# Performance work log

Measured on AMD Instinct MI355X. Metric: run time of the kernel, lower is better.

Reference implementation:

```python
import jax, jax.numpy as jnp
import numpy as np

B, S, D = 4, 2048, 1024
H = 16
HD = D // H  # 64


def setup_inputs() -> dict:
    key = jax.random.key(0)
    ks = jax.random.split(key, 8)
    scale = 1.0 / np.sqrt(D)
    return {
        "hidden_states": jax.random.normal(ks[0], (B, S, D), dtype=jnp.float32),
        "attention_mask": jnp.ones((B, 1, 1, S), dtype=jnp.int32),
        "Wq": jax.random.normal(ks[1], (D, D), dtype=jnp.float32) * scale,
        "bq": jax.random.normal(ks[2], (D,), dtype=jnp.float32) * 0.02,
        "Wk": jax.random.normal(ks[3], (D, D), dtype=jnp.float32) * scale,
        "bk": jax.random.normal(ks[4], (D,), dtype=jnp.float32) * 0.02,
        "Wv": jax.random.normal(ks[5], (D, D), dtype=jnp.float32) * scale,
        "bv": jax.random.normal(ks[6], (D,), dtype=jnp.float32) * 0.02,
    }


def _split_heads(x):
    # [b, t, (h d)] -> [b, h, t, d]
    b, t, _ = x.shape
    return x.reshape(b, t, H, HD).transpose(0, 2, 1, 3)


def reference(hidden_states, attention_mask, Wq, bq, Wk, bk, Wv, bv):
    # Linear projections (torch Linear: x @ W.T + b)
    q = _split_heads(hidden_states @ Wq.T + bq)
    k = _split_heads(hidden_states @ Wk.T + bk)
    v = _split_heads(hidden_states @ Wv.T + bv)

    # scaled dot-product scores: [b, h, s, s]
    scores = jnp.einsum("bhqd,bhkd->bhqk", q, k) / np.sqrt(HD)

    s = scores.shape[-1]
    causal = jnp.tril(jnp.ones((s, s), dtype=bool))[None, None]
    neg_inf = jnp.float32(-jnp.inf)
    scores = jnp.where(causal, scores, neg_inf)
    # attention_mask is 0/1 keep mask: [b, 1, 1, s]
    scores = jnp.where(attention_mask == 0, neg_inf, scores)

    probs = jax.nn.softmax(scores, axis=-1)  # dropout p=0 (eval)
    ctx = jnp.einsum("bhqk,bhkd->bhqd", probs, v)
    # [b, h, t, d] -> [b, t, h*d]
    return ctx.transpose(0, 2, 1, 3).reshape(hidden_states.shape[0], s, D)
```

## Files before the change

kernel.cpp:

```cpp
#include <hip/hip_runtime.h>
#include <hip/hip_bf16.h>
#include <math.h>


#define B_ 4
#define S_ 2048
#define D_ 1024
#define H_ 16
#define HD_ 64
#define M_ (B_ * S_)

typedef unsigned short u16;
typedef unsigned int u32;
typedef __attribute__((ext_vector_type(4))) float f32x4;
typedef __attribute__((ext_vector_type(8))) short bf16x8;

__device__ __forceinline__ u16 f2bfu_rn(float x) {
    u32 u = __builtin_bit_cast(u32, x);
    return (u16)((u + 0x8000u) >> 16);
}

__device__ __forceinline__ void gl2lds16(const void* g, void* l) {
    __builtin_amdgcn_global_load_lds(
        (const __attribute__((address_space(1))) u32*)g,
        (__attribute__((address_space(3))) u32*)l, 16, 0, 0);
}

#define XN  8388608u
#define WN  1048576u
__global__ __launch_bounds__(256) void convert_bf16(
    const float* __restrict__ X,  const float* __restrict__ Wq,
    const float* __restrict__ Wk, const float* __restrict__ Wv,
    u16* __restrict__ Xb, u16* __restrict__ Wqb,
    u16* __restrict__ Wkb, u16* __restrict__ Wvb)
{
    size_t idx = ((size_t)blockIdx.x * 256 + threadIdx.x) * 8;
    const float* src; u16* dst; size_t off;
    if (idx < XN)                { src = X;  dst = Xb;  off = idx; }
    else if (idx < XN + WN)      { src = Wq; dst = Wqb; off = idx - XN; }
    else if (idx < XN + 2 * WN)  { src = Wk; dst = Wkb; off = idx - XN - WN; }
    else                         { src = Wv; dst = Wvb; off = idx - XN - 2 * WN; }
    float4 a = *(const float4*)(src + off);
    float4 b = *(const float4*)(src + off + 4);
    uint4 o;
    o.x = (u32)f2bfu_rn(a.x) | ((u32)f2bfu_rn(a.y) << 16);
    o.y = (u32)f2bfu_rn(a.z) | ((u32)f2bfu_rn(a.w) << 16);
    o.z = (u32)f2bfu_rn(b.x) | ((u32)f2bfu_rn(b.y) << 16);
    o.w = (u32)f2bfu_rn(b.z) | ((u32)f2bfu_rn(b.w) << 16);
    *(uint4*)(dst + off) = o;
}

#define QSCALE 0.18033688011112042f

__global__ __launch_bounds__(256) void qkv_mfma(
    const u16* __restrict__ Xb,
    const u16* __restrict__ Wqb, const u16* __restrict__ Wkb,
    const u16* __restrict__ Wvb,
    const float* __restrict__ bq, const float* __restrict__ bk,
    const float* __restrict__ bv,
    u16* __restrict__ Qb, u16* __restrict__ Kb, u16* __restrict__ Vtb)
{
    const int which = blockIdx.z;
    const u16* Asrc; const u16* Bsrc; const float* bias; u16* Out;
    int m0, n0;
    if (which == 0)      { Asrc = Xb;  Bsrc = Wqb; bias = bq; Out = Qb;
                           m0 = blockIdx.y * 128; n0 = blockIdx.x * 128; }
    else if (which == 1) { Asrc = Xb;  Bsrc = Wkb; bias = bk; Out = Kb;
                           m0 = blockIdx.y * 128; n0 = blockIdx.x * 128; }
    else                 { Asrc = Wvb; Bsrc = Xb;  bias = bv; Out = Vtb;
                           m0 = blockIdx.x * 128; n0 = blockIdx.y * 128; }

    __shared__ u16 As[128][64];
    __shared__ u16 Bs[128][64];

    const int t = threadIdx.x;
    const int wave = t >> 6, lane = t & 63;
    const int qd = lane >> 4, l15 = lane & 15;
    const int wm = wave >> 1, wn = wave & 1;

    const f32x4 zero = {0.f, 0.f, 0.f, 0.f};
    f32x4 acc[4][4];
#pragma unroll
    for (int i = 0; i < 4; ++i)
#pragma unroll
        for (int j = 0; j < 4; ++j) acc[i][j] = zero;

    for (int k0 = 0; k0 < D_; k0 += 64) {
        __syncthreads();
#pragma unroll
        for (int i = 0; i < 4; ++i) {
            int r0  = (wave * 4 + i) * 8;
            int row = r0 + (lane >> 3);
            int g   = (lane & 7) ^ (row & 7);
            gl2lds16(Asrc + (size_t)(m0 + row) * D_ + k0 + g * 8, &As[r0][0]);
            gl2lds16(Bsrc + (size_t)(n0 + row) * D_ + k0 + g * 8, &Bs[r0][0]);
        }
        __syncthreads();
#pragma unroll
        for (int ks = 0; ks < 2; ++ks) {
            bf16x8 af[4], bf[4];
#pragma unroll
            for (int mt = 0; mt < 4; ++mt) {
                int row = wm * 64 + mt * 16 + l15;
                int p = (ks * 4 + qd) ^ (row & 7);
                af[mt] = *(const bf16x8*)&As[row][p * 8];
            }
#pragma unroll
            for (int nt = 0; nt < 4; ++nt) {
                int row = wn * 64 + nt * 16 + l15;
                int p = (ks * 4 + qd) ^ (row & 7);
                bf[nt] = *(const bf16x8*)&Bs[row][p * 8];
            }
#pragma unroll
            for (int mt = 0; mt < 4; ++mt)
#pragma unroll
                for (int nt = 0; nt < 4; ++nt)
                    acc[mt][nt] = __builtin_amdgcn_mfma_f32_16x16x32_bf16(
                        af[mt], bf[nt], acc[mt][nt], 0, 0, 0);
        }
    }

    if (which < 2) {
#pragma unroll
        for (int nt = 0; nt < 4; ++nt) {
            int n = n0 + wn * 64 + nt * 16 + l15;
            float bv_ = bias[n];
            int h = n >> 6, hd = n & 63;
#pragma unroll
            for (int mt = 0; mt < 4; ++mt)
#pragma unroll
                for (int r = 0; r < 4; ++r) {
                    int m = m0 + wm * 64 + mt * 16 + qd * 4 + r;
                    int bb = m >> 11, s = m & 2047;
                    float v = acc[mt][nt][r] + bv_;
                    if (which == 0) v *= QSCALE;
                    Out[(((size_t)(bb * H_ + h)) * S_ + s) * HD_ + hd] = f2bfu_rn(v);
                }
        }
    } else {
#pragma unroll
        for (int mt = 0; mt < 4; ++mt)
#pragma unroll
            for (int r = 0; r < 4; ++r) {
                int f = m0 + wm * 64 + mt * 16 + qd * 4 + r;
                float bv_ = bias[f];
                int h = f >> 6, hd = f & 63;
#pragma unroll
                for (int nt = 0; nt < 4; ++nt) {
                    int tok = n0 + wn * 64 + nt * 16 + l15;
                    int bb = tok >> 11, s = tok & 2047;
                    float v = acc[mt][nt][r] + bv_;
                    Out[(((size_t)(bb * H_ + h)) * HD_ + hd) * S_ + s] = f2bfu_rn(v);
                }
            }
    }
}

__global__ __launch_bounds__(256) void attn_mfma(
    const u16* __restrict__ Qb, const u16* __restrict__ Kb,
    const u16* __restrict__ Vtb, const int* __restrict__ amask,
    float* __restrict__ Out)
{
    const int bh = blockIdx.y;
    const int b = bh >> 4, h = bh & 15;
    const int qt = (int)(gridDim.x - 1) - (int)blockIdx.x;
    const int q0 = qt * 64;
    const int t = threadIdx.x;
    const int wave = t >> 6, lane = t & 63;
    const int qd = lane >> 4, l15 = lane & 15;

    __shared__ u16 Ks[64][64];
    __shared__ u16 Vts[64][64];
    __shared__ u16 Ps[64][72];
    __shared__ float mb[64];

    const size_t base = (size_t)bh * S_ * HD_;
    const u16* Qg = Qb + base;
    const u16* Kg = Kb + base;
    const u16* Vg = Vtb + base;

    bf16x8 qf[2];
    {
        const u16* qrow = Qg + (size_t)(q0 + wave * 16 + l15) * HD_;
        qf[0] = *(const bf16x8*)(qrow + qd * 8);
        qf[1] = *(const bf16x8*)(qrow + 32 + qd * 8);
    }
    bf16x8 onesf;
    {
        short v = (l15 == 0) ? (short)0x3F80 : (short)0;
        onesf = (bf16x8){v, v, v, v, v, v, v, v};
    }

    const f32x4 zero = {0.f, 0.f, 0.f, 0.f};
    f32x4 o[5];
#pragma unroll
    for (int i = 0; i < 5; ++i) o[i] = zero;

    for (int jt = 0; jt <= qt; ++jt) {
        const int j0 = jt * 64;
        __syncthreads();
#pragma unroll
        for (int i = 0; i < 2; ++i) {
            int r0  = (wave * 2 + i) * 8;
            int row = r0 + (lane >> 3);
            int g   = (lane & 7) ^ (row & 7);
            gl2lds16(Kg + (size_t)(j0 + row) * HD_ + g * 8, &Ks[r0][0]);
            gl2lds16(Vg + (size_t)row * S_ + j0 + g * 8, &Vts[r0][0]);
        }
        if (t < 64) mb[t] = (amask[b * S_ + j0 + t] == 0) ? -1e30f : 0.0f;
        __syncthreads();

        f32x4 sacc[4];
#pragma unroll
        for (int nt = 0; nt < 4; ++nt) sacc[nt] = zero;
#pragma unroll
        for (int ks = 0; ks < 2; ++ks) {
#pragma unroll
            for (int nt = 0; nt < 4; ++nt) {
                int brow = nt * 16 + l15;
                int bp = (ks * 4 + qd) ^ (brow & 7);
                bf16x8 bf = *(const bf16x8*)&Ks[brow][bp * 8];
                sacc[nt] = __builtin_amdgcn_mfma_f32_16x16x32_bf16(
                    qf[ks], bf, sacc[nt], 0, 0, 0);
            }
        }

        float bias[4];
#pragma unroll
        for (int nt = 0; nt < 4; ++nt) bias[nt] = mb[nt * 16 + l15];
        const bool diag = (jt == qt);
#pragma unroll
        for (int r = 0; r < 4; ++r) {
            int prow = wave * 16 + qd * 4 + r;
#pragma unroll
            for (int nt = 0; nt < 4; ++nt) {
                int col = nt * 16 + l15;
                float s = sacc[nt][r] + bias[nt];
                if (diag && col > (prow)) s = -1e30f;
                float p = __builtin_amdgcn_exp2f(s);
                Ps[prow][col] = f2bfu_rn(p);
            }
        }

#pragma unroll
        for (int ks = 0; ks < 2; ++ks) {
            int arow = wave * 16 + l15;
            bf16x8 pf = *(const bf16x8*)&Ps[arow][ks * 32 + qd * 8];
#pragma unroll
            for (int nt = 0; nt < 4; ++nt) {
                int brow = nt * 16 + l15;
                int bp = (ks * 4 + qd) ^ (brow & 7);
                bf16x8 vf = *(const bf16x8*)&Vts[brow][bp * 8];
                o[nt] = __builtin_amdgcn_mfma_f32_16x16x32_bf16(
                    pf, vf, o[nt], 0, 0, 0);
            }
            o[4] = __builtin_amdgcn_mfma_f32_16x16x32_bf16(
                pf, onesf, o[4], 0, 0, 0);
        }
    }

#pragma unroll
    for (int r = 0; r < 4; ++r) {
        float l = __shfl(o[4][r], lane & 48);
        float inv = 1.0f / l;
        int q = q0 + wave * 16 + qd * 4 + r;
#pragma unroll
        for (int nt = 0; nt < 4; ++nt) {
            int hd = nt * 16 + l15;
            Out[((size_t)(b * S_ + q)) * D_ + h * HD_ + hd] = o[nt][r] * inv;
        }
    }
}

extern "C" void kernel_launch(void* const* d_in, const int* in_sizes, int n_in,
                              void* d_out, int out_size, void* d_ws, size_t ws_size,
                              hipStream_t stream) {
    (void)in_sizes; (void)n_in; (void)out_size; (void)ws_size;
    const float* X    = (const float*)d_in[0];
    const int*   mask = (const int*)d_in[1];
    const float* Wq   = (const float*)d_in[2];
    const float* bq   = (const float*)d_in[3];
    const float* Wk   = (const float*)d_in[4];
    const float* bk   = (const float*)d_in[5];
    const float* Wv   = (const float*)d_in[6];
    const float* bv   = (const float*)d_in[7];
    float* out = (float*)d_out;

    u16* Xb  = (u16*)d_ws;
    u16* Wqb = Xb  + XN;
    u16* Wkb = Wqb + WN;
    u16* Wvb = Wkb + WN;
    u16* Qb  = Wvb + WN;
    u16* Kb  = Qb  + XN;
    u16* Vtb = Kb  + XN;

    convert_bf16<<<(XN + 3 * WN) / (256 * 8), 256, 0, stream>>>(
        X, Wq, Wk, Wv, Xb, Wqb, Wkb, Wvb);
    qkv_mfma<<<dim3(D_ / 128, M_ / 128, 3), 256, 0, stream>>>(
        Xb, Wqb, Wkb, Wvb, bq, bk, bv, Qb, Kb, Vtb);
    attn_mfma<<<dim3(S_ / 64, B_ * H_), 256, 0, stream>>>(
        Qb, Kb, Vtb, mask, out);
}
```

Before: 281.8 us.

## Load weights directly into registers in QKV GEMM; use 32x32 MFMA 128-row attention tiles

The QKV projection kernel no longer stages the weight tile in shared memory. Each wave loads its weight fragments straight from global memory into registers, and only the token tile goes through LDS; the V path swaps the MFMA operand order to keep its transposed output. The attention kernel now processes 128 query rows per block using 32x32x16 MFMA instructions, so each K/V tile loaded into LDS is reused by twice as many queries. This cuts LDS traffic and block count, at the cost of uncoalesced global weight loads and more causal-masked work on diagonal tiles.

```diff
diff --git a/kernel.cpp b/kernel.cpp
--- a/kernel.cpp
+++ b/kernel.cpp
@@ -13,6 +13,7 @@
 typedef unsigned short u16;
 typedef unsigned int u32;
 typedef __attribute__((ext_vector_type(4))) float f32x4;
+typedef __attribute__((ext_vector_type(16))) float f32x16;
 typedef __attribute__((ext_vector_type(8))) short bf16x8;
 
 __device__ __forceinline__ u16 f2bfu_rn(float x) {
@@ -61,22 +62,20 @@
     u16* __restrict__ Qb, u16* __restrict__ Kb, u16* __restrict__ Vtb)
 {
     const int which = blockIdx.z;
-    const u16* Asrc; const u16* Bsrc; const float* bias; u16* Out;
-    int m0, n0;
-    if (which == 0)      { Asrc = Xb;  Bsrc = Wqb; bias = bq; Out = Qb;
-                           m0 = blockIdx.y * 128; n0 = blockIdx.x * 128; }
-    else if (which == 1) { Asrc = Xb;  Bsrc = Wkb; bias = bk; Out = Kb;
-                           m0 = blockIdx.y * 128; n0 = blockIdx.x * 128; }
-    else                 { Asrc = Wvb; Bsrc = Xb;  bias = bv; Out = Vtb;
-                           m0 = blockIdx.x * 128; n0 = blockIdx.y * 128; }
-
-    __shared__ u16 As[128][64];
-    __shared__ u16 Bs[128][64];
+    const u16* __restrict__ W = (which == 0) ? Wqb : (which == 1) ? Wkb : Wvb;
+    const float* __restrict__ bias = (which == 0) ? bq : (which == 1) ? bk : bv;
+    u16* __restrict__ Out = (which == 0) ? Qb : (which == 1) ? Kb : Vtb;
+
+    const int ft0 = blockIdx.x * 128;
+    const int tt0 = blockIdx.y * 128;
+
+    __shared__ u16 Xs[128][64];
 
     const int t = threadIdx.x;
     const int wave = t >> 6, lane = t & 63;
     const int qd = lane >> 4, l15 = lane & 15;
-    const int wm = wave >> 1, wn = wave & 1;
+    const int wl = wave >> 1;
+    const int wg = wave & 1;
 
     const f32x4 zero = {0.f, 0.f, 0.f, 0.f};
     f32x4 acc[4][4];
@@ -92,64 +91,75 @@
             int r0  = (wave * 4 + i) * 8;
             int row = r0 + (lane >> 3);
             int g   = (lane & 7) ^ (row & 7);
-            gl2lds16(Asrc + (size_t)(m0 + row) * D_ + k0 + g * 8, &As[r0][0]);
-            gl2lds16(Bsrc + (size_t)(n0 + row) * D_ + k0 + g * 8, &Bs[r0][0]);
-        }
+            gl2lds16(Xb + (size_t)(tt0 + row) * D_ + k0 + g * 8, &Xs[r0][0]);
+        }
+        bf16x8 wf[2][4];
+#pragma unroll
+        for (int ks = 0; ks < 2; ++ks)
+#pragma unroll
+            for (int gt = 0; gt < 4; ++gt)
+                wf[ks][gt] = *(const bf16x8*)&W[
+                    (size_t)(ft0 + wg * 64 + gt * 16 + l15) * D_ +
+                    k0 + ks * 32 + qd * 8];
         __syncthreads();
+
 #pragma unroll
         for (int ks = 0; ks < 2; ++ks) {
-            bf16x8 af[4], bf[4];
-#pragma unroll
-            for (int mt = 0; mt < 4; ++mt) {
-                int row = wm * 64 + mt * 16 + l15;
+            bf16x8 xf[4];
+#pragma unroll
+            for (int lt = 0; lt < 4; ++lt) {
+                int row = wl * 64 + lt * 16 + l15;
                 int p = (ks * 4 + qd) ^ (row & 7);
-                af[mt] = *(const bf16x8*)&As[row][p * 8];
+                xf[lt] = *(const bf16x8*)&Xs[row][p * 8];
             }
-#pragma unroll
-            for (int nt = 0; nt < 4; ++nt) {
-                int row = wn * 64 + nt * 16 + l15;
-                int p = (ks * 4 + qd) ^ (row & 7);
-                bf[nt] = *(const bf16x8*)&Bs[row][p * 8];
+            if (which < 2) {
+#pragma unroll
+                for (int lt = 0; lt < 4; ++lt)
+#pragma unroll
+                    for (int gt = 0; gt < 4; ++gt)
+                        acc[lt][gt] = __builtin_amdgcn_mfma_f32_16x16x32_bf16(
+                            xf[lt], wf[ks][gt], acc[lt][gt], 0, 0, 0);
+            } else {
+#pragma unroll
+                for (int lt = 0; lt < 4; ++lt)
+#pragma unroll
+                    for (int gt = 0; gt < 4; ++gt)
+                        acc[lt][gt] = __builtin_amdgcn_mfma_f32_16x16x32_bf16(
+                            wf[ks][gt], xf[lt], acc[lt][gt], 0, 0, 0);
             }
-#pragma unroll
-            for (int mt = 0; mt < 4; ++mt)
-#pragma unroll
-                for (int nt = 0; nt < 4; ++nt)
-                    acc[mt][nt] = __builtin_amdgcn_mfma_f32_16x16x32_bf16(
-                        af[mt], bf[nt], acc[mt][nt], 0, 0, 0);
         }
     }
 
     if (which < 2) {
 #pragma unroll
-        for (int nt = 0; nt < 4; ++nt) {
-            int n = n0 + wn * 64 + nt * 16 + l15;
+        for (int gt = 0; gt < 4; ++gt) {
+            int n = ft0 + wg * 64 + gt * 16 + l15;
             float bv_ = bias[n];
             int h = n >> 6, hd = n & 63;
 #pragma unroll
-            for (int mt = 0; mt < 4; ++mt)
+            for (int lt = 0; lt < 4; ++lt)
 #pragma unroll
                 for (int r = 0; r < 4; ++r) {
-                    int m = m0 + wm * 64 + mt * 16 + qd * 4 + r;
+                    int m = tt0 + wl * 64 + lt * 16 + qd * 4 + r;
                     int bb = m >> 11, s = m & 2047;
-                    float v = acc[mt][nt][r] + bv_;
+                    float v = acc[lt][gt][r] + bv_;
                     if (which == 0) v *= QSCALE;
                     Out[(((size_t)(bb * H_ + h)) * S_ + s) * HD_ + hd] = f2bfu_rn(v);
                 }
         }
     } else {
 #pragma unroll
-        for (int mt = 0; mt < 4; ++mt)
+        for (int gt = 0; gt < 4; ++gt)
 #pragma unroll
             for (int r = 0; r < 4; ++r) {
-                int f = m0 + wm * 64 + mt * 16 + qd * 4 + r;
+                int f = ft0 + wg * 64 + gt * 16 + qd * 4 + r;
                 float bv_ = bias[f];
                 int h = f >> 6, hd = f & 63;
 #pragma unroll
-                for (int nt = 0; nt < 4; ++nt) {
-                    int tok = n0 + wn * 64 + nt * 16 + l15;
+                for (int lt = 0; lt < 4; ++lt) {
+                    int tok = tt0 + wl * 64 + lt * 16 + l15;
                     int bb = tok >> 11, s = tok & 2047;
-                    float v = acc[mt][nt][r] + bv_;
+                    float v = acc[gt < 0 ? 0 : lt][gt][r] + bv_;
                     Out[(((size_t)(bb * H_ + h)) * HD_ + hd) * S_ + s] = f2bfu_rn(v);
                 }
             }
@@ -164,14 +174,14 @@
     const int bh = blockIdx.y;
     const int b = bh >> 4, h = bh & 15;
     const int qt = (int)(gridDim.x - 1) - (int)blockIdx.x;
-    const int q0 = qt * 64;
+    const int q0 = qt * 128;
     const int t = threadIdx.x;
     const int wave = t >> 6, lane = t & 63;
-    const int qd = lane >> 4, l15 = lane & 15;
+    const int l31 = lane & 31, half = lane >> 5;
 
     __shared__ u16 Ks[64][64];
     __shared__ u16 Vts[64][64];
-    __shared__ u16 Ps[64][72];
+    __shared__ u16 Ps[128][64];
     __shared__ float mb[64];
 
     const size_t base = (size_t)bh * S_ * HD_;
@@ -179,24 +189,25 @@
     const u16* Kg = Kb + base;
     const u16* Vg = Vtb + base;
 
-    bf16x8 qf[2];
+    const int qrow_w = wave * 32;
+
+    bf16x8 qf[4];
     {
-        const u16* qrow = Qg + (size_t)(q0 + wave * 16 + l15) * HD_;
-        qf[0] = *(const bf16x8*)(qrow + qd * 8);
-        qf[1] = *(const bf16x8*)(qrow + 32 + qd * 8);
+        const u16* qp = Qg + (size_t)(q0 + qrow_w + l31) * HD_ + half * 8;
+#pragma unroll
+        for (int kc = 0; kc < 4; ++kc) qf[kc] = *(const bf16x8*)(qp + kc * 16);
     }
     bf16x8 onesf;
     {
-        short v = (l15 == 0) ? (short)0x3F80 : (short)0;
+        short v = (l31 == 0) ? (short)0x3F80 : (short)0;
         onesf = (bf16x8){v, v, v, v, v, v, v, v};
     }
 
-    const f32x4 zero = {0.f, 0.f, 0.f, 0.f};
-    f32x4 o[5];
-#pragma unroll
-    for (int i = 0; i < 5; ++i) o[i] = zero;
-
-    for (int jt = 0; jt <= qt; ++jt) {
+    f32x16 o0 = {0.f,0.f,0.f,0.f,0.f,0.f,0.f,0.f,0.f,0.f,0.f,0.f,0.f,0.f,0.f,0.f};
+    f32x16 o1 = o0, lacc = o0;
+
+    const int nT = 2 * qt + 2;
+    for (int jt = 0; jt < nT; ++jt) {
         const int j0 = jt * 64;
         __syncthreads();
 #pragma unroll
@@ -210,65 +221,63 @@
         if (t < 64) mb[t] = (amask[b * S_ + j0 + t] == 0) ? -1e30f : 0.0f;
         __syncthreads();
 
-        f32x4 sacc[4];
-#pragma unroll
-        for (int nt = 0; nt < 4; ++nt) sacc[nt] = zero;
-#pragma unroll
-        for (int ks = 0; ks < 2; ++ks) {
-#pragma unroll
-            for (int nt = 0; nt < 4; ++nt) {
-                int brow = nt * 16 + l15;
-                int bp = (ks * 4 + qd) ^ (brow & 7);
-                bf16x8 bf = *(const bf16x8*)&Ks[brow][bp * 8];
-                sacc[nt] = __builtin_amdgcn_mfma_f32_16x16x32_bf16(
-                    qf[ks], bf, sacc[nt], 0, 0, 0);
+        f32x16 s0 = {0.f,0.f,0.f,0.f,0.f,0.f,0.f,0.f,0.f,0.f,0.f,0.f,0.f,0.f,0.f,0.f};
+        f32x16 s1 = s0;
+#pragma unroll
+        for (int kc = 0; kc < 4; ++kc) {
+            int gr = kc * 2 + half;
+            int p0 = gr ^ (l31 & 7);
+            bf16x8 k0f = *(const bf16x8*)&Ks[l31][p0 * 8];
+            bf16x8 k1f = *(const bf16x8*)&Ks[32 + l31][p0 * 8];
+            s0 = __builtin_amdgcn_mfma_f32_32x32x16_bf16(qf[kc], k0f, s0, 0, 0, 0);
+            s1 = __builtin_amdgcn_mfma_f32_32x32x16_bf16(qf[kc], k1f, s1, 0, 0, 0);
+        }
+
+        const float bias0 = mb[l31], bias1 = mb[32 + l31];
+        const bool diag = (j0 + 63 > q0 + qrow_w);
+#pragma unroll
+        for (int reg = 0; reg < 16; ++reg) {
+            int row  = (reg & 3) + 8 * (reg >> 2) + 4 * half;
+            int prow = qrow_w + row;
+            int q    = q0 + prow;
+            float sA = s0[reg] + bias0;
+            float sB = s1[reg] + bias1;
+            if (diag) {
+                if (j0 + l31 > q)      sA = -1e30f;
+                if (j0 + 32 + l31 > q) sB = -1e30f;
             }
-        }
-
-        float bias[4];
-#pragma unroll
-        for (int nt = 0; nt < 4; ++nt) bias[nt] = mb[nt * 16 + l15];
-        const bool diag = (jt == qt);
-#pragma unroll
-        for (int r = 0; r < 4; ++r) {
-            int prow = wave * 16 + qd * 4 + r;
-#pragma unroll
-            for (int nt = 0; nt < 4; ++nt) {
-                int col = nt * 16 + l15;
-                float s = sacc[nt][r] + bias[nt];
-                if (diag && col > (prow)) s = -1e30f;
-                float p = __builtin_amdgcn_exp2f(s);
-                Ps[prow][col] = f2bfu_rn(p);
-            }
-        }
-
-#pragma unroll
-        for (int ks = 0; ks < 2; ++ks) {
-            int arow = wave * 16 + l15;
-            bf16x8 pf = *(const bf16x8*)&Ps[arow][ks * 32 + qd * 8];
-#pragma unroll
-            for (int nt = 0; nt < 4; ++nt) {
-                int brow = nt * 16 + l15;
-                int bp = (ks * 4 + qd) ^ (brow & 7);
-                bf16x8 vf = *(const bf16x8*)&Vts[brow][bp * 8];
-                o[nt] = __builtin_amdgcn_mfma_f32_16x16x32_bf16(
-                    pf, vf, o[nt], 0, 0, 0);
-            }
-            o[4] = __builtin_amdgcn_mfma_f32_16x16x32_bf16(
-                pf, onesf, o[4], 0, 0, 0);
-        }
-    }
-
-#pragma unroll
-    for (int r = 0; r < 4; ++r) {
-        float l = __shfl(o[4][r], lane & 48);
+            float pA = __builtin_amdgcn_exp2f(sA);
+            float pB = __builtin_amdgcn_exp2f(sB);
+            int gA = (l31 >> 3) ^ (prow & 7);
+            int gB = (4 + (l31 >> 3)) ^ (prow & 7);
+            Ps[prow][gA * 8 + (l31 & 7)] = f2bfu_rn(pA);
+            Ps[prow][gB * 8 + (l31 & 7)] = f2bfu_rn(pB);
+        }
+
+#pragma unroll
+        for (int kc = 0; kc < 4; ++kc) {
+            int gr = kc * 2 + half;
+            int prow = qrow_w + l31;
+            int pp = gr ^ (prow & 7);
+            bf16x8 pf = *(const bf16x8*)&Ps[prow][pp * 8];
+            int vp = gr ^ (l31 & 7);
+            bf16x8 v0f = *(const bf16x8*)&Vts[l31][vp * 8];
+            bf16x8 v1f = *(const bf16x8*)&Vts[32 + l31][vp * 8];
+            o0 = __builtin_amdgcn_mfma_f32_32x32x16_bf16(pf, v0f, o0, 0, 0, 0);
+            o1 = __builtin_amdgcn_mfma_f32_32x32x16_bf16(pf, v1f, o1, 0, 0, 0);
+            lacc = __builtin_amdgcn_mfma_f32_32x32x16_bf16(pf, onesf, lacc, 0, 0, 0);
+        }
+    }
+
+#pragma unroll
+    for (int reg = 0; reg < 16; ++reg) {
+        float l = __shfl(lacc[reg], lane & 32);
         float inv = 1.0f / l;
-        int q = q0 + wave * 16 + qd * 4 + r;
-#pragma unroll
-        for (int nt = 0; nt < 4; ++nt) {
-            int hd = nt * 16 + l15;
-            Out[((size_t)(b * S_ + q)) * D_ + h * HD_ + hd] = o[nt][r] * inv;
-        }
+        int row = (reg & 3) + 8 * (reg >> 2) + 4 * half;
+        int q = q0 + qrow_w + row;
+        float* op = Out + ((size_t)(b * S_ + q)) * D_ + h * HD_;
+        op[l31]      = o0[reg] * inv;
+        op[32 + l31] = o1[reg] * inv;
     }
 }
 
@@ -298,6 +307,6 @@
         X, Wq, Wk, Wv, Xb, Wqb, Wkb, Wvb);
     qkv_mfma<<<dim3(D_ / 128, M_ / 128, 3), 256, 0, stream>>>(
         Xb, Wqb, Wkb, Wvb, bq, bk, bv, Qb, Kb, Vtb);
-    attn_mfma<<<dim3(S_ / 64, B_ * H_), 256, 0, stream>>>(
+    attn_mfma<<<dim3(S_ / 128, B_ * H_), 256, 0, stream>>>(
         Qb, Kb, Vtb, mask, out);
 }
```

Result: slower. 352.3 us (+25.0%).
